# Kernel tuning notes

Hardware: AMD Instinct MI355X
Metric: run time of the kernel (lower is better)

## Reference

```python
import jax, jax.numpy as jnp
import numpy as np

B, T, E = 2, 2048, 2048
H, NOPE, ROPE, VD, KVR, DR = 16, 64, 32, 64, 256, 2
QKD = NOPE + ROPE  # 96
LOWR = KVR // 4    # hypernet low_rank=4 -> 64


def _rope_angles(position, dim):
    # freqs_cis angles: pos * 10000^(-2i/dim), matching torch rotary with theta=10000
    inv = jnp.exp(jnp.arange(0, dim, 2, dtype=jnp.float32) * (-jnp.log(jnp.float32(10000.0)) / dim))
    return position.astype(jnp.float32)[..., None] * inv  # (1, T, dim//2)


def _apply_rotary(x, ang):
    # x: (B,T,H,D); pairs are consecutive elements (view_as_complex semantics)
    x2 = x.reshape(x.shape[:-1] + (-1, 2))
    c = jnp.cos(ang)[:, :, None, :]
    s = jnp.sin(ang)[:, :, None, :]
    xr, xi = x2[..., 0], x2[..., 1]
    return jnp.stack([xr * c - xi * s, xr * s + xi * c], axis=-1).reshape(x.shape)


def _layernorm(x, g, b, eps=1e-5):
    m = jnp.mean(x, axis=-1, keepdims=True)
    v = jnp.var(x, axis=-1, keepdims=True)
    return (x - m) * jax.lax.rsqrt(v + eps) * g + b


def _sinusoid_pe(t, d):
    pos = jnp.arange(t, dtype=jnp.float32)[:, None]
    div = jnp.exp(jnp.arange(0, d, 2, dtype=jnp.float32) * (-jnp.log(jnp.float32(10000.0)) / d))
    pe = jnp.zeros((t, d), dtype=jnp.float32)
    pe = pe.at[:, 0::2].set(jnp.sin(pos * div)).at[:, 1::2].set(jnp.cos(pos * div))
    return pe


def setup_inputs() -> dict:
    key = jax.random.key(0)
    ks = jax.random.split(key, 16)
    sd = 0.02
    return {
        "query": jax.random.normal(ks[0], (B, T, E), jnp.float32),
        "key": jax.random.normal(ks[1], (B, T, E), jnp.float32),
        "value": jax.random.normal(ks[2], (B, T, E), jnp.float32),
        "position": jnp.arange(T, dtype=jnp.int32)[None, :],
        # weights stored transposed for right-multiply (x @ W)
        "wq": jax.random.normal(ks[3], (E, H * QKD), jnp.float32) * sd,
        "wkv_a": jax.random.normal(ks[4], (E, KVR + ROPE), jnp.float32) * sd,
        "kv_gamma": jnp.ones((KVR,), jnp.float32),
        "kv_beta": jnp.zeros((KVR,), jnp.float32),
        # torch layout (H*(NOPE+VD), KVR) kept for faithful view(H,-1,KVR) absorb
        "wkv_b": jax.random.normal(ks[5], (H * (NOPE + VD), KVR), jnp.float32) * sd,
        "wo": jax.random.normal(ks[6], (H * VD, E), jnp.float32) * sd,
        "fc_c_w": jax.random.normal(ks[7], (KVR, LOWR), jnp.float32) * sd,
        "fc_c_b": jnp.zeros((LOWR,), jnp.float32),
        "fc_p_w": jax.random.normal(ks[8], (KVR, LOWR), jnp.float32) * sd,
        "fc_p_b": jnp.zeros((LOWR,), jnp.float32),
    }


def reference(query, key, value, position, wq, wkv_a, kv_gamma, kv_beta, wkv_b, wo,
              fc_c_w, fc_c_b, fc_p_w, fc_p_b):
    bsz, seqlen, _ = query.shape
    # queries: low-rank-free path (q_lora_rank=0)
    q = (query @ wq).reshape(bsz, seqlen, H, QKD)
    q_nope, q_pe = q[..., :NOPE], q[..., NOPE:]
    ang = _rope_angles(position, ROPE)  # (1, T, ROPE//2)
    q_pe = _apply_rotary(q_pe, ang[:, -seqlen:])
    # key/value latent projection
    kv_all = key @ wkv_a  # (B, T, KVR+ROPE)
    kv, k_pe = kv_all[..., :KVR], kv_all[..., KVR:]
    k_pe = _apply_rotary(k_pe[:, :, None, :], ang)[:, :, 0, :]  # (B, T, ROPE)
    kv_norm = _layernorm(kv, kv_gamma, kv_beta)  # (B, T, KVR)
    # hypernetwork temporal downsampling weights (train path, T_input=kv_norm)
    t = -(-seqlen // DR)
    C = jnp.repeat(_sinusoid_pe(t, KVR), DR, axis=0)[:seqlen]  # (T, KVR)
    C2 = C @ fc_c_w + fc_c_b           # (T, LOWR)
    P2 = kv_norm @ fc_p_w + fc_p_b     # (B, T, LOWR)
    W = jax.nn.sigmoid(jnp.einsum('tc,bsc->bts', C2, P2))  # (B, T, T)
    idx = jnp.arange(seqlen)
    chunk = idx // DR
    # chunk mask: cumulative within-chunk causal accumulation
    zero_mask = ((chunk[:, None] == chunk[None, :]) & (idx[None, :] <= idx[:, None])).astype(query.dtype)
    kv_t = jnp.einsum('bts,bsc->btc', W * zero_mask, kv_norm)  # (B, T, KVR)
    # stride-aware causal mask: attend completed chunk-end slots + own in-progress slot
    allowed = (idx[None, :] == idx[:, None]) | ((idx[None, :] < idx[:, None]) & (((idx[None, :] + 1) % DR) == 0))
    attn_mask = jnp.where(allowed, jnp.float32(0.0), jnp.float32(-1e30))
    # absorbed MLA attention
    wb = wkv_b.reshape(H, NOPE + VD, KVR)
    q_abs = jnp.einsum('bshd,hdc->bshc', q_nope, wb[:, :NOPE])  # (B, S, H, KVR)
    scores = (jnp.einsum('bshc,btc->bsht', q_abs, kv_t)
              + jnp.einsum('bshr,btr->bsht', q_pe, k_pe)) * (QKD ** -0.5)
    scores = scores + attn_mask[None, :, None, :]
    attn = jax.nn.softmax(scores, axis=-1)
    x = jnp.einsum('bsht,btc->bshc', attn, kv_t)
    x = jnp.einsum('bshc,hdc->bshd', x, wb[:, NOPE:])  # (B, S, H, VD)
    return x.reshape(bsz, seqlen, H * VD) @ wo
```

## Files before the change

kernel.cpp:

```cpp
#include <hip/hip_runtime.h>
#include <stddef.h>

typedef unsigned short u16;
typedef unsigned short u16x8 __attribute__((ext_vector_type(8)));
typedef short s16x8 __attribute__((ext_vector_type(8)));
typedef float f32x4 __attribute__((ext_vector_type(4)));

#define B_ 2
#define T_ 2048
#define E_ 2048
#define H_ 16

__device__ inline float us2f(u16 u){
  unsigned int i = ((unsigned int)u) << 16;
  return __builtin_bit_cast(float, i);
}
__device__ inline u16 f2us(float f){
  unsigned int x = __builtin_bit_cast(unsigned int, f);
  unsigned int r = (x + 0x7fffu + ((x >> 16) & 1u)) >> 16;
  return (u16)r;
}
__device__ inline f32x4 mfma32(s16x8 a, s16x8 b, f32x4 c){
  return __builtin_amdgcn_mfma_f32_16x16x32_bf16(a, b, c, 0, 0, 0);
}
__device__ inline s16x8 ld8(const u16* p){
  return __builtin_bit_cast(s16x8, *(const u16x8*)p);
}
__device__ inline void gload_lds16(const u16* g, u16* l){
  __builtin_amdgcn_global_load_lds(
      (const __attribute__((address_space(1))) unsigned int*)(g),
      (__attribute__((address_space(3))) unsigned int*)(l), 16, 0, 0);
}

__global__ __launch_bounds__(256) void prep_cvt(
    const float* __restrict__ wq, const float* __restrict__ wkva,
    const float* __restrict__ wo, const float* __restrict__ wkvb,
    const float* __restrict__ query, const float* __restrict__ key_,
    u16* __restrict__ wqT, u16* __restrict__ wkvaT, u16* __restrict__ woT,
    u16* __restrict__ wkvbB, u16* __restrict__ queryB, u16* __restrict__ keyB)
{
  __shared__ float tile[32][33];
  const int bid = blockIdx.x;
  const int tid = threadIdx.x;
  if (bid < 5696) {
    const float* in; u16* out; int R, C, bx, by;
    if (bid < 3072)      { in = wq;   out = wqT;   R = 2048; C = 1536; bx = bid % 48;          by = bid / 48; }
    else if (bid < 3648) { in = wkva; out = wkvaT; R = 2048; C = 288;  bx = (bid-3072) % 9;    by = (bid-3072) / 9; }
    else                 { in = wo;   out = woT;   R = 1024; C = 2048; bx = (bid-3648) % 64;   by = (bid-3648) / 64; }
    int tx = tid & 31, ty = tid >> 5;
    int c0 = bx * 32, r0 = by * 32;
    for (int i = ty; i < 32; i += 8){
      int r = r0 + i, c = c0 + tx;
      tile[i][tx] = (r < R && c < C) ? in[(size_t)r * C + c] : 0.f;
    }
    __syncthreads();
    for (int i = ty; i < 32; i += 8){
      int c = c0 + i, r = r0 + tx;
      if (c < C && r < R) out[(size_t)c * R + r] = f2us(tile[tx][i]);
    }
  } else if (bid < 6208) {
    int i = (bid - 5696) * 1024 + tid * 4;
    f32x4 v = *(const f32x4*)(wkvb + i);
    wkvbB[i]   = f2us(v[0]); wkvbB[i+1] = f2us(v[1]);
    wkvbB[i+2] = f2us(v[2]); wkvbB[i+3] = f2us(v[3]);
  } else {
    const int n_each = 4096 * 2048;
    int idx = (bid - 6208) * 1024 + tid * 4;
    const float* in; u16* out; int i;
    if (idx < n_each){ in = query; out = queryB; i = idx; }
    else             { in = key_;  out = keyB;   i = idx - n_each; }
    if (i + 3 < n_each){
      f32x4 v = *(const f32x4*)(in + i);
      out[i]   = f2us(v[0]); out[i+1] = f2us(v[1]);
      out[i+2] = f2us(v[2]); out[i+3] = f2us(v[3]);
    }
  }
}

__global__ __launch_bounds__(256) void proj2(
    const u16* __restrict__ queryB, const u16* __restrict__ wqT, u16* __restrict__ qp,
    const u16* __restrict__ keyB, const u16* __restrict__ wkvaT, u16* __restrict__ kvall)
{
  __shared__ __align__(16) u16 smem[16384];
  const int bid = blockIdx.x;
  const int tid  = threadIdx.x;
  const int lane = tid & 63;
  const int wid  = tid >> 6;
  const int quad = lane >> 4;
  const int col  = lane & 15;

  if (bid < 768) {
    const int N = 1536, K = 2048, Klen = 1024;
    const int swz = (bid & 7) * 96 + (bid >> 3);
    const int kh  = swz / 384;
    const int rem = swz % 384;
    const int bm = (rem / 12) * 128;
    const int bn = (rem % 12) * 128;
    const int waveM = wid >> 1, waveN = wid & 1;
    u16* As = smem;
    u16* Bs = smem + 8192;

    const int srow = wid * 16 + (lane >> 2);
    const int scol = (lane & 3) * 8;
    const u16* ga = queryB + (size_t)(bm + srow) * K + kh * Klen + scol;
    const u16* gb = wqT    + (size_t)(bn + srow) * K + kh * Klen + scol;
    const size_t rowskip = (size_t)64 * K;
    u16* Cp = qp + (size_t)kh * 4096 * N;

    f32x4 acc[4][4] = {};
    const int nt = Klen >> 5;

    auto STAGE = [&](int buf, int kk){
      u16* la = &As[buf * 4096 + wid * 512];
      u16* lb = &Bs[buf * 4096 + wid * 512];
      gload_lds16(ga + kk,           la);
      gload_lds16(ga + rowskip + kk, la + 2048);
      gload_lds16(gb + kk,           lb);
      gload_lds16(gb + rowskip + kk, lb + 2048);
    };

    STAGE(0, 0);
    asm volatile("s_waitcnt vmcnt(0)" ::: "memory");
    __builtin_amdgcn_s_barrier();
    __builtin_amdgcn_sched_barrier(0);

    int cur = 0;
    for (int it = 0; it < nt; ++it){
      if (it + 1 < nt) STAGE(cur ^ 1, (it + 1) * 32);
      const u16* as = &As[cur * 4096];
      const u16* bs = &Bs[cur * 4096];
      s16x8 af[4], bf[4];
#pragma unroll
      for (int i = 0; i < 4; ++i) af[i] = ld8(&as[(waveM*64 + i*16 + col) * 32 + quad*8]);
#pragma unroll
      for (int i = 0; i < 4; ++i) bf[i] = ld8(&bs[(waveN*64 + i*16 + col) * 32 + quad*8]);
#pragma unroll
      for (int i = 0; i < 4; ++i)
#pragma unroll
        for (int j = 0; j < 4; ++j)
          acc[i][j] = mfma32(af[i], bf[j], acc[i][j]);
      asm volatile("s_waitcnt lgkmcnt(0)" ::: "memory");
      if (it + 1 < nt)
        asm volatile("s_waitcnt vmcnt(0)" ::: "memory");
      __builtin_amdgcn_s_barrier();
      __builtin_amdgcn_sched_barrier(0);
      cur ^= 1;
    }
#pragma unroll
    for (int i = 0; i < 4; ++i)
#pragma unroll
      for (int j = 0; j < 4; ++j)
#pragma unroll
        for (int r = 0; r < 4; ++r) {
          int row = bm + waveM*64 + i*16 + quad*4 + r;
          int c   = bn + waveN*64 + j*16 + col;
          Cp[(size_t)row * N + c] = f2us(acc[i][j][r]);
        }
  } else {
    const int N = 288, K = 2048;
    const int r_ = bid - 768;
    const int bm = (r_ / 5) * 64;
    const int bn = (r_ % 5) * 64;
    const int lr = tid >> 2;
    const int lc = (tid & 3) * 8;
    const int waveM = wid >> 1, waveN = wid & 1;
    u16* As = smem;
    u16* Bs = smem + 2560;

    f32x4 acc[2][2];
    for (int i = 0; i < 2; ++i)
      for (int j = 0; j < 2; ++j)
        acc[i][j] = (f32x4){0.f, 0.f, 0.f, 0.f};

    const u16x8 zero8 = {0,0,0,0,0,0,0,0};
    const bool bok = (bn + lr) < N;
    const u16* arow = keyB  + (size_t)(bm + lr) * K + lc;
    const u16* brow = wkvaT + (size_t)(bn + lr) * K + lc;

    for (int kk = 0; kk < K; kk += 32) {
      u16x8 av = *(const u16x8*)(arow + kk);
      u16x8 bv = bok ? *(const u16x8*)(brow + kk) : zero8;
      __syncthreads();
      *(u16x8*)&As[lr*40 + lc] = av;
      *(u16x8*)&Bs[lr*40 + lc] = bv;
      __syncthreads();
      s16x8 af0 = ld8(&As[(waveM*32 + col)*40 + quad*8]);
      s16x8 af1 = ld8(&As[(waveM*32 + 16 + col)*40 + quad*8]);
      s16x8 bf0 = ld8(&Bs[(waveN*32 + col)*40 + quad*8]);
      s16x8 bf1 = ld8(&Bs[(waveN*32 + 16 + col)*40 + quad*8]);
      acc[0][0] = mfma32(af0, bf0, acc[0][0]);
      acc[0][1] = mfma32(af0, bf1, acc[0][1]);
      acc[1][0] = mfma32(af1, bf0, acc[1][0]);
      acc[1][1] = mfma32(af1, bf1, acc[1][1]);
    }
    for (int am = 0; am < 2; ++am)
      for (int bnn = 0; bnn < 2; ++bnn)
        for (int i = 0; i < 4; ++i) {
          int r = bm + waveM*32 + am*16 + quad*4 + i;
          int c = bn + waveN*32 + bnn*16 + col;
          if (c < N) kvall[(size_t)r * N + c] = f2us(acc[am][bnn][i]);
        }
  }
}

template<int OUT_F32>
__global__ __launch_bounds__(256) void gemm128(const u16* __restrict__ A,
    const u16* __restrict__ Bt, void* __restrict__ Cp, int M, int N, int K, int gx)
{
  __shared__ __align__(16) u16 As[2 * 128 * 32];
  __shared__ __align__(16) u16 Bs[2 * 128 * 32];
  const int lin = blockIdx.x;
  const int cpx = gridDim.x >> 3;
  const int swz = (lin & 7) * cpx + (lin >> 3);
  const int bxi = swz % gx;
  const int byi = swz / gx;
  const int tid  = threadIdx.x;
  const int lane = tid & 63;
  const int wid  = tid >> 6;
  const int quad = lane >> 4;
  const int col  = lane & 15;
  const int bm = byi * 128;
  const int bn = bxi * 128;
  const int waveM = wid >> 1, waveN = wid & 1;

  const int srow = wid * 16 + (lane >> 2);
  const int scol = (lane & 3) * 8;
  const u16* ga = A  + (size_t)(bm + srow) * K + scol;
  const u16* gb = Bt + (size_t)(bn + srow) * K + scol;
  const size_t rowskip = (size_t)64 * K;

  f32x4 acc[4][4] = {};
  const int nt = K >> 5;

  auto STAGE = [&](int buf, int kk){
    u16* la = &As[buf * 4096 + wid * 512];
    u16* lb = &Bs[buf * 4096 + wid * 512];
    gload_lds16(ga + kk,           la);
    gload_lds16(ga + rowskip + kk, la + 2048);
    gload_lds16(gb + kk,           lb);
    gload_lds16(gb + rowskip + kk, lb + 2048);
  };

  STAGE(0, 0);
  asm volatile("s_waitcnt vmcnt(0)" ::: "memory");
  __builtin_amdgcn_s_barrier();
  __builtin_amdgcn_sched_barrier(0);

  int cur = 0;
  for (int it = 0; it < nt; ++it){
    if (it + 1 < nt) STAGE(cur ^ 1, (it + 1) * 32);
    const u16* as = &As[cur * 4096];
    const u16* bs = &Bs[cur * 4096];
    s16x8 af[4], bf[4];
#pragma unroll
    for (int i = 0; i < 4; ++i) af[i] = ld8(&as[(waveM*64 + i*16 + col) * 32 + quad*8]);
#pragma unroll
    for (int i = 0; i < 4; ++i) bf[i] = ld8(&bs[(waveN*64 + i*16 + col) * 32 + quad*8]);
#pragma unroll
    for (int i = 0; i < 4; ++i)
#pragma unroll
      for (int j = 0; j < 4; ++j)
        acc[i][j] = mfma32(af[i], bf[j], acc[i][j]);
    asm volatile("s_waitcnt lgkmcnt(0)" ::: "memory");
    if (it + 1 < nt)
      asm volatile("s_waitcnt vmcnt(0)" ::: "memory");
    __builtin_amdgcn_s_barrier();
    __builtin_amdgcn_sched_barrier(0);
    cur ^= 1;
  }
#pragma unroll
  for (int i = 0; i < 4; ++i)
#pragma unroll
    for (int j = 0; j < 4; ++j)
#pragma unroll
      for (int r = 0; r < 4; ++r) {
        int row = bm + waveM*64 + i*16 + quad*4 + r;
        int c   = bn + waveN*64 + j*16 + col;
        if (OUT_F32) ((float*)Cp)[(size_t)row * N + c] = acc[i][j][r];
        else         ((u16*)Cp)[(size_t)row * N + c]   = f2us(acc[i][j][r]);
      }
}

__global__ __launch_bounds__(256) void mid3(
    const u16* __restrict__ qp, const int* __restrict__ pos, u16* __restrict__ qh,
    const u16* __restrict__ kvall, const float* __restrict__ gamma,
    const float* __restrict__ beta, const float* __restrict__ fcpw,
    const float* __restrict__ fcpb, u16* __restrict__ kvn,
    float* __restrict__ P2, u16* __restrict__ kpe,
    const float* __restrict__ fccw, const float* __restrict__ fccb,
    float* __restrict__ C2)
{
  __shared__ float fsm[520];
  const int bid = blockIdx.x;
  const int tid = threadIdx.x;

  if (bid < 3072) {
    const size_t PS = 4096ull * 1536;
    int idx = bid * 256 + tid;
    int c    = idx % 12;
    int rest = idx / 12;
    int h    = rest & 15;
    int row  = rest >> 4;
    int t    = row & (T_ - 1);
    int b    = row >> 11;
    size_t off = (size_t)row * 1536 + h * 96 + c * 8;
    u16x8 v0 = *(const u16x8*)(qp + off);
    u16x8 v1 = *(const u16x8*)(qp + PS + off);
    u16x8 v;
    if (c < 8) {
#pragma unroll
      for (int k = 0; k < 8; ++k) v[k] = f2us(us2f(v0[k]) + us2f(v1[k]));
    } else {
      int i0 = (c - 8) * 4;
      float pp = (float)pos[t];
#pragma unroll
      for (int k = 0; k < 4; ++k){
        int i = i0 + k;
        float ang = pp * __expf((float)(2*i) * -0.28782313657f);
        float cs = __cosf(ang), sn = __sinf(ang);
        float xr = us2f(v0[2*k])   + us2f(v1[2*k]);
        float xi = us2f(v0[2*k+1]) + us2f(v1[2*k+1]);
        v[2*k]   = f2us(xr * cs - xi * sn);
        v[2*k+1] = f2us(xr * sn + xi * cs);
      }
    }
    u16* dst = qh + ((size_t)(b * 16 + h) * T_ + t) * 96;
    *(u16x8*)(dst + c * 8) = v;
  } else if (bid < 7168) {
    const int row = bid - 3072;
    const int lane = tid & 63, wid = tid >> 6;
    float* kvs   = fsm;
    float* part  = fsm + 256;
    float* redS  = fsm + 512;
    float* redS2 = fsm + 516;
    const u16* src = kvall + (size_t)row * 288;
    float v = us2f(src[tid]);
    float s1 = v, s2 = v * v;
    for (int off = 1; off < 64; off <<= 1){
      s1 += __shfl_xor(s1, off);
      s2 += __shfl_xor(s2, off);
    }
    if (lane == 0){ redS[wid] = s1; redS2[wid] = s2; }
    __syncthreads();
    float S  = redS[0] + redS[1] + redS[2] + redS[3];
    float Q  = redS2[0] + redS2[1] + redS2[2] + redS2[3];
    float mean = S * (1.f / 256.f);
    float var  = Q * (1.f / 256.f) - mean * mean;
    float rstd = rsqrtf(var + 1e-5f);
    float xn = (v - mean) * rstd * gamma[tid] + beta[tid];
    kvs[tid] = xn;
    kvn[(size_t)row * 256 + tid] = f2us(xn);
    __syncthreads();
    {
      int oc = tid & 63, pp = tid >> 6;
      float acc = 0.f;
#pragma unroll 8
      for (int c = pp * 64; c < pp * 64 + 64; ++c)
        acc += kvs[c] * fcpw[c * 64 + oc];
      part[tid] = acc;
    }
    __syncthreads();
    if (tid < 64) {
      P2[(size_t)row * 64 + tid] = fcpb[tid] + part[tid] + part[64 + tid]
                                 + part[128 + tid] + part[192 + tid];
    } else if (tid < 80) {
      int i = tid - 64;
      int t = row & (T_ - 1);
      float ang = (float)pos[t] * __expf((float)(2*i) * -0.28782313657f);
      float c = __cosf(ang), s = __sinf(ang);
      float xr = us2f(src[256 + 2*i]);
      float xi = us2f(src[257 + 2*i]);
      kpe[(size_t)row * 32 + 2*i]     = f2us(xr * c - xi * s);
      kpe[(size_t)row * 32 + 2*i + 1] = f2us(xr * s + xi * c);
    }
  } else {
    const int t = bid - 7168;
    float* pe   = fsm;
    float* part = fsm + 256;
    float p = (float)(t >> 1);
    if (tid < 128){
      float div = __expf((float)(2*tid) * -0.03597789207f);
      float a = p * div;
      pe[2*tid]   = __sinf(a);
      pe[2*tid+1] = __cosf(a);
    }
    __syncthreads();
    {
      int oc = tid & 63, pp = tid >> 6;
      float acc = 0.f;
#pragma unroll 8
      for (int c = pp * 64; c < pp * 64 + 64; ++c)
        acc += pe[c] * fccw[c * 64 + oc];
      part[tid] = acc;
    }
    __syncthreads();
    if (tid < 64)
      C2[t * 64 + tid] = fccb[tid] + part[tid] + part[64 + tid]
                       + part[128 + tid] + part[192 + tid];
  }
}

__global__ __launch_bounds__(256) void kvt_kernel(const float* __restrict__ C2,
    const float* __restrict__ P2, const u16* __restrict__ kvn, u16* __restrict__ kvt)
{
  const int row = blockIdx.x * 4 + (threadIdx.x >> 6);
  const int lane = threadIdx.x & 63;
  const int t = row & (T_ - 1);
  float c2v = C2[t * 64 + lane];
  float da = c2v * P2[(size_t)row * 64 + lane];
  for (int off = 1; off < 64; off <<= 1) da += __shfl_xor(da, off);
  float wtt = 1.f / (1.f + __expf(-da));
  const bool odd = (t & 1);
  float wts = 0.f;
  if (odd){
    float db = c2v * P2[(size_t)(row - 1) * 64 + lane];
    for (int off = 1; off < 64; off <<= 1) db += __shfl_xor(db, off);
    wts = 1.f / (1.f + __expf(-db));
  }
  for (int c = lane; c < 256; c += 64){
    float val = wtt * us2f(kvn[(size_t)row * 256 + c]);
    if (odd) val += wts * us2f(kvn[(size_t)(row - 1) * 256 + c]);
    kvt[(size_t)row * 256 + c] = f2us(val);
  }
}

__global__ __launch_bounds__(256) void vtkc_kernel(const u16* __restrict__ kvb,
    const u16* __restrict__ kpe, u16* __restrict__ Vt, u16* __restrict__ Kc)
{
  __shared__ __align__(16) u16 tile[64][72];
  const int tid = threadIdx.x;
  if (blockIdx.x < 512) {
    const int bid = blockIdx.x;
    const int jt = bid & 15;
    const int h  = (bid >> 4) & 15;
    const int b  = bid >> 8;
    const int jl = tid >> 2;
    const int dseg = (tid & 3) * 16;
    const int j0 = jt * 64;
    {
      int s_ = 2 * (j0 + jl) + 1;
      const u16* src = kvb + ((size_t)(b * T_ + s_)) * 2048 + h * 128 + 64 + dseg;
      *(u16x8*)&tile[jl][dseg]     = *(const u16x8*)(src);
      *(u16x8*)&tile[jl][dseg + 8] = *(const u16x8*)(src + 8);
    }
    __syncthreads();
    const int dl = tid >> 2;
    const int jseg = (tid & 3) * 16;
    u16* dst = Vt + ((size_t)(b * 16 + h) * 64 + dl) * 1024 + j0 + jseg;
    u16x8 o;
    for (int r = 0; r < 8; ++r) o[r] = tile[jseg + r][dl];
    *(u16x8*)dst = o;
    for (int r = 0; r < 8; ++r) o[r] = tile[jseg + 8 + r][dl];
    *(u16x8*)(dst + 8) = o;
  } else {
    int idx = (blockIdx.x - 512) * 256 + tid;
    int c  = idx % 12;
    int j  = (idx / 12) & 1023;
    int bh = idx / (12 * 1024);
    if (bh >= B_ * H_) return;
    int b = bh >> 4, h = bh & 15;
    int t = 2 * j + 1;
    u16x8 v;
    if (c < 8) v = *(const u16x8*)(kvb + ((size_t)(b * T_ + t)) * 2048 + h * 128 + c * 8);
    else       v = *(const u16x8*)(kpe + ((size_t)(b * T_ + t)) * 32 + (c - 8) * 8);
    int kl = j & 63;
    int cs = (c & 12) | ((c & 3) ^ ((kl >> 1) & 3));
    *(u16x8*)(Kc + ((size_t)bh * 1024 + j) * 96 + cs * 8) = v;
  }
}

__global__ __launch_bounds__(256) void attn_kernel(
    const u16* __restrict__ qh, const u16* __restrict__ kvb,
    const u16* __restrict__ kpe, const u16* __restrict__ Kc,
    const u16* __restrict__ Vt, u16* __restrict__ xout)
{
  __shared__ __align__(16) u16 Ks[64 * 96];
  __shared__ __align__(16) u16 Vs[64][72];
  __shared__ __align__(16) u16 pbufA[4][16 * 72];
  const int tid  = threadIdx.x;
  const int wid  = tid >> 6;
  const int lane = tid & 63;
  const int quad = lane >> 4;
  const int col  = lane & 15;
  const int qt   = 31 - (blockIdx.x >> 5);
  const int bh   = blockIdx.x & 31;
  const int b    = bh >> 4;
  const int h    = bh & 15;
  u16* pbuf = pbufA[wid];
  const float scale = 0.10206207262f;
  const u16* KcH = Kc + (size_t)bh * 1024 * 96;
  const u16* VtH = Vt + (size_t)bh * 64 * 1024;
  const int t0 = qt * 64 + wid * 16;
  const int qo = (quad * 8) ^ (((col >> 1) & 3) << 3);

  s16x8 aq0, aq1, aq2;
  {
    const u16* qrow = qh + ((size_t)bh * T_ + t0 + col) * 96;
    aq0 = ld8(qrow + quad * 8);
    aq1 = ld8(qrow + 32 + quad * 8);
    aq2 = ld8(qrow + 64 + quad * 8);
  }
  float sself;
  {
    const int t = t0 + col;
    const u16* qrow = qh + ((size_t)bh * T_ + t) * 96;
    const u16* ka = kvb + ((size_t)(b * T_ + t)) * 2048 + h * 128;
    const u16* kp = kpe + ((size_t)(b * T_ + t)) * 32;
    float a = 0.f;
#pragma unroll
    for (int c = 0; c < 8; ++c){
      u16x8 qv = *(const u16x8*)(qrow + c * 8);
      u16x8 kv = *(const u16x8*)(ka + c * 8);
#pragma unroll
      for (int jj = 0; jj < 8; ++jj) a += us2f(qv[jj]) * us2f(kv[jj]);
    }
#pragma unroll
    for (int c = 0; c < 4; ++c){
      u16x8 qv = *(const u16x8*)(qrow + 64 + c * 8);
      u16x8 kv = *(const u16x8*)(kp + c * 8);
#pragma unroll
      for (int jj = 0; jj < 8; ++jj) a += us2f(qv[jj]) * us2f(kv[jj]);
    }
    sself = a * scale;
  }
  float es[4], lacc[4];
  f32x4 O[4];
#pragma unroll
  for (int i = 0; i < 4; ++i){
    es[i] = __expf(__shfl(sself, quad * 4 + i));
    lacc[i] = 0.f;
  }
#pragma unroll
  for (int nt = 0; nt < 4; ++nt)
#pragma unroll
    for (int i = 0; i < 4; ++i){
      int t = t0 + quad * 4 + i;
      O[nt][i] = es[i] * us2f(kvb[((size_t)(b * T_ + t)) * 2048 + h * 128 + 64 + nt * 16 + col]);
    }

  const int nb = (qt * 32 + 94) >> 6;
  for (int blk = 0; blk < nb; ++blk) {
    const int jb = blk * 64;
    __syncthreads();
    {
      const u16* gk = KcH + (size_t)jb * 96 + (wid * 3) * 512 + lane * 8;
      u16* lk = &Ks[(wid * 3) * 512];
#pragma unroll
      for (int k = 0; k < 3; ++k)
        gload_lds16(gk + k * 512, lk + k * 512);
      int d = tid >> 2, c4 = tid & 3;
      const u16* gv = VtH + (size_t)d * 1024 + jb + c4 * 16;
      u16* lv = &Vs[d][c4 * 16];
      *(u16x8*)(lv)     = *(const u16x8*)(gv);
      *(u16x8*)(lv + 8) = *(const u16x8*)(gv + 8);
    }
    __syncthreads();
#pragma unroll
    for (int cc = 0; cc < 2; ++cc){
      const u16* k0 = &Ks[(cc * 32 + col) * 96];
      const u16* k1 = k0 + 16 * 96;
      f32x4 s0 = {0,0,0,0}, s1 = {0,0,0,0};
      s0 = mfma32(aq0, ld8(k0 + qo), s0);
      s0 = mfma32(aq1, ld8(k0 + 32 + qo), s0);
      s0 = mfma32(aq2, ld8(k0 + 64 + qo), s0);
      s1 = mfma32(aq0, ld8(k1 + qo), s1);
      s1 = mfma32(aq1, ld8(k1 + 32 + qo), s1);
      s1 = mfma32(aq2, ld8(k1 + 64 + qo), s1);
      int key0 = jb + cc * 32 + col;
#pragma unroll
      for (int i = 0; i < 4; ++i){
        int lim = (t0 + quad * 4 + i) >> 1;
        float p0 = (key0 < lim)      ? __expf(s0[i] * scale) : 0.f;
        float p1 = (key0 + 16 < lim) ? __expf(s1[i] * scale) : 0.f;
        lacc[i] += p0 + p1;
        pbuf[(quad * 4 + i) * 72 + cc * 32 + col]      = f2us(p0);
        pbuf[(quad * 4 + i) * 72 + cc * 32 + 16 + col] = f2us(p1);
      }
    }
    asm volatile("s_waitcnt lgkmcnt(0)" ::: "memory");
    __builtin_amdgcn_sched_barrier(0);
#pragma unroll
    for (int cc = 0; cc < 2; ++cc){
      s16x8 pf = ld8(&pbuf[col * 72 + cc * 32 + quad * 8]);
#pragma unroll
      for (int nt = 0; nt < 4; ++nt)
        O[nt] = mfma32(pf, ld8(&Vs[nt * 16 + col][cc * 32 + quad * 8]), O[nt]);
    }
  }
#pragma unroll
  for (int i = 0; i < 4; ++i){
    float l = lacc[i];
    l += __shfl_xor(l, 1);
    l += __shfl_xor(l, 2);
    l += __shfl_xor(l, 4);
    l += __shfl_xor(l, 8);
    lacc[i] = es[i] + l;
  }
#pragma unroll
  for (int nt = 0; nt < 4; ++nt)
#pragma unroll
    for (int i = 0; i < 4; ++i){
      int t = t0 + quad * 4 + i;
      xout[((size_t)(b * T_ + t)) * 1024 + h * 64 + nt * 16 + col] = f2us(O[nt][i] / lacc[i]);
    }
}

extern "C" void kernel_launch(void* const* d_in, const int* in_sizes, int n_in,
                              void* d_out, int out_size, void* d_ws, size_t ws_size,
                              hipStream_t stream)
{
  (void)in_sizes; (void)n_in; (void)out_size; (void)ws_size;
  const float* query = (const float*)d_in[0];
  const float* key_  = (const float*)d_in[1];
  const int*   pos   = (const int*)d_in[3];
  const float* wq    = (const float*)d_in[4];
  const float* wkva  = (const float*)d_in[5];
  const float* gamma = (const float*)d_in[6];
  const float* beta  = (const float*)d_in[7];
  const float* wkvb  = (const float*)d_in[8];
  const float* wo    = (const float*)d_in[9];
  const float* fccw  = (const float*)d_in[10];
  const float* fccb  = (const float*)d_in[11];
  const float* fcpw  = (const float*)d_in[12];
  const float* fcpb  = (const float*)d_in[13];

  char* p = (char*)d_ws;
  auto alloc = [&](size_t bytes) -> void* {
    void* r = (void*)p;
    p += (bytes + 255) & ~(size_t)255;
    return r;
  };
  u16* wqT    = (u16*)alloc(1536ull * 2048 * 2);
  u16* wkvaT  = (u16*)alloc(288ull  * 2048 * 2);
  u16* woT    = (u16*)alloc(2048ull * 1024 * 2);
  u16* wkvbB  = (u16*)alloc(2048ull * 256 * 2);
  u16* queryB = (u16*)alloc(4096ull * 2048 * 2);
  u16* keyB   = (u16*)alloc(4096ull * 2048 * 2);
  u16* qp     = (u16*)alloc(2ull * 4096 * 1536 * 2);
  u16* qh     = (u16*)alloc(65536ull * 96 * 2);
  u16* kvall  = (u16*)alloc(4096ull * 288 * 2);
  u16* kvn    = (u16*)alloc(4096ull * 256 * 2);
  u16* kpe    = (u16*)alloc(4096ull * 32 * 2);
  float* P2   = (float*)alloc(4096ull * 64 * 4);
  float* C2   = (float*)alloc(2048ull * 64 * 4);
  u16* kvt    = (u16*)alloc(4096ull * 256 * 2);
  u16* kvb    = (u16*)alloc(4096ull * 2048 * 2);
  char* q8 = (char*)qp;
  u16* Kc = (u16*)q8;
  u16* Vt = (u16*)(q8 + ((32ull*1024*96*2 + 255) & ~255ull));
  u16* x  = (u16*)(q8 + ((32ull*1024*96*2 + 255) & ~255ull)
                      + ((2048ull*1024*2   + 255) & ~255ull));

  prep_cvt<<<22592, 256, 0, stream>>>(wq, wkva, wo, wkvb, query, key_,
                                      wqT, wkvaT, woT, wkvbB, queryB, keyB);
  proj2<<<1088, 256, 0, stream>>>(queryB, wqT, qp, keyB, wkvaT, kvall);
  mid3<<<9216, 256, 0, stream>>>(qp, pos, qh, kvall, gamma, beta, fcpw, fcpb,
                                 kvn, P2, kpe, fccw, fccb, C2);
  kvt_kernel<<<1024, 256, 0, stream>>>(C2, P2, kvn, kvt);

  gemm128<0><<<512, 256, 0, stream>>>(kvt, wkvbB, kvb, 4096, 2048, 256, 16);
  vtkc_kernel<<<2048, 256, 0, stream>>>(kvb, kpe, Vt, Kc);
  attn_kernel<<<1024, 256, 0, stream>>>(qh, kvb, kpe, Kc, Vt, x);

  gemm128<1><<<512, 256, 0, stream>>>(x, woT, d_out, 4096, 2048, 1024, 16);
}
```

Before: 337.3 us.

## Split-K the kv_a projection into four fp32 partials and interleave blocks with q projection

The small key×wkv_a GEMM used to run 320 blocks, each looping over the full K=2048. It now uses a 4-way split-K with fp32 partial outputs, which mid3 sums when it loads. Block ids are remapped so q-projection tiles and kv tiles interleave across the grid, the q tiles get an M-grouped ordering, MFMA sections get higher wave priority, and the kv loop prefetches the next global tile into registers. This targets the long tail from the serial kv blocks, at the cost of extra fp32 partial traffic and summation work in mid3.

```diff
diff --git a/kernel.cpp b/kernel.cpp
--- a/kernel.cpp
+++ b/kernel.cpp
@@ -79,7 +79,7 @@
 
 __global__ __launch_bounds__(256) void proj2(
     const u16* __restrict__ queryB, const u16* __restrict__ wqT, u16* __restrict__ qp,
-    const u16* __restrict__ keyB, const u16* __restrict__ wkvaT, u16* __restrict__ kvall)
+    const u16* __restrict__ keyB, const u16* __restrict__ wkvaT, float* __restrict__ kvp)
 {
   __shared__ __align__(16) u16 smem[16384];
   const int bid = blockIdx.x;
@@ -88,14 +88,19 @@
   const int wid  = tid >> 6;
   const int quad = lane >> 4;
   const int col  = lane & 15;
-
-  if (bid < 768) {
+  const int g  = bid >> 3;
+  const int e  = bid & 7;
+  const int gm = g & 7;
+
+  if (gm < 3) {
+    const int id = e * 96 + (g >> 3) * 3 + gm;
+    const int kh   = id / 384;
+    const int r2   = id % 384;
+    const int bmHi = r2 / 48;
+    const int r3   = r2 % 48;
+    const int bn = (r3 >> 2) * 128;
+    const int bm = (bmHi * 4 + (r3 & 3)) * 128;
     const int N = 1536, K = 2048, Klen = 1024;
-    const int swz = (bid & 7) * 96 + (bid >> 3);
-    const int kh  = swz / 384;
-    const int rem = swz % 384;
-    const int bm = (rem / 12) * 128;
-    const int bn = (rem % 12) * 128;
     const int waveM = wid >> 1, waveN = wid & 1;
     u16* As = smem;
     u16* Bs = smem + 8192;
@@ -134,11 +139,13 @@
       for (int i = 0; i < 4; ++i) af[i] = ld8(&as[(waveM*64 + i*16 + col) * 32 + quad*8]);
 #pragma unroll
       for (int i = 0; i < 4; ++i) bf[i] = ld8(&bs[(waveN*64 + i*16 + col) * 32 + quad*8]);
+      __builtin_amdgcn_s_setprio(1);
 #pragma unroll
       for (int i = 0; i < 4; ++i)
 #pragma unroll
         for (int j = 0; j < 4; ++j)
           acc[i][j] = mfma32(af[i], bf[j], acc[i][j]);
+      __builtin_amdgcn_s_setprio(0);
       asm volatile("s_waitcnt lgkmcnt(0)" ::: "memory");
       if (it + 1 < nt)
         asm volatile("s_waitcnt vmcnt(0)" ::: "memory");
@@ -157,10 +164,12 @@
           Cp[(size_t)row * N + c] = f2us(acc[i][j][r]);
         }
   } else {
-    const int N = 288, K = 2048;
-    const int r_ = bid - 768;
-    const int bm = (r_ / 5) * 64;
-    const int bn = (r_ % 5) * 64;
+    const int id = e * 160 + (g >> 3) * 5 + (gm - 3);
+    const int kh = id / 320;
+    const int r  = id % 320;
+    const int bm = (r / 5) * 64;
+    const int bn = (r % 5) * 64;
+    const int N = 288, K = 2048, Klen = 512;
     const int lr = tid >> 2;
     const int lc = (tid & 3) * 8;
     const int waveM = wid >> 1, waveN = wid & 1;
@@ -174,15 +183,20 @@
 
     const u16x8 zero8 = {0,0,0,0,0,0,0,0};
     const bool bok = (bn + lr) < N;
-    const u16* arow = keyB  + (size_t)(bm + lr) * K + lc;
-    const u16* brow = wkvaT + (size_t)(bn + lr) * K + lc;
-
-    for (int kk = 0; kk < K; kk += 32) {
-      u16x8 av = *(const u16x8*)(arow + kk);
-      u16x8 bv = bok ? *(const u16x8*)(brow + kk) : zero8;
+    const u16* arow = keyB  + (size_t)(bm + lr) * K + kh * Klen + lc;
+    const u16* brow = wkvaT + (size_t)(bn + lr) * K + kh * Klen + lc;
+    float* Cp = kvp + (size_t)kh * 4096 * N;
+
+    u16x8 av = *(const u16x8*)(arow);
+    u16x8 bv = bok ? *(const u16x8*)(brow) : zero8;
+    for (int kk = 0; kk < Klen; kk += 32) {
       __syncthreads();
       *(u16x8*)&As[lr*40 + lc] = av;
       *(u16x8*)&Bs[lr*40 + lc] = bv;
+      if (kk + 32 < Klen){
+        av = *(const u16x8*)(arow + kk + 32);
+        bv = bok ? *(const u16x8*)(brow + kk + 32) : zero8;
+      }
       __syncthreads();
       s16x8 af0 = ld8(&As[(waveM*32 + col)*40 + quad*8]);
       s16x8 af1 = ld8(&As[(waveM*32 + 16 + col)*40 + quad*8]);
@@ -196,9 +210,9 @@
     for (int am = 0; am < 2; ++am)
       for (int bnn = 0; bnn < 2; ++bnn)
         for (int i = 0; i < 4; ++i) {
-          int r = bm + waveM*32 + am*16 + quad*4 + i;
-          int c = bn + waveN*32 + bnn*16 + col;
-          if (c < N) kvall[(size_t)r * N + c] = f2us(acc[am][bnn][i]);
+          int rr = bm + waveM*32 + am*16 + quad*4 + i;
+          int c  = bn + waveN*32 + bnn*16 + col;
+          if (c < N) Cp[(size_t)rr * N + c] = acc[am][bnn][i];
         }
   }
 }
@@ -283,7 +297,7 @@
 
 __global__ __launch_bounds__(256) void mid3(
     const u16* __restrict__ qp, const int* __restrict__ pos, u16* __restrict__ qh,
-    const u16* __restrict__ kvall, const float* __restrict__ gamma,
+    const float* __restrict__ kvp, const float* __restrict__ gamma,
     const float* __restrict__ beta, const float* __restrict__ fcpw,
     const float* __restrict__ fcpb, u16* __restrict__ kvn,
     float* __restrict__ P2, u16* __restrict__ kpe,
@@ -329,12 +343,13 @@
   } else if (bid < 7168) {
     const int row = bid - 3072;
     const int lane = tid & 63, wid = tid >> 6;
+    const size_t PSk = 4096ull * 288;
     float* kvs   = fsm;
     float* part  = fsm + 256;
     float* redS  = fsm + 512;
     float* redS2 = fsm + 516;
-    const u16* src = kvall + (size_t)row * 288;
-    float v = us2f(src[tid]);
+    const float* src = kvp + (size_t)row * 288;
+    float v = (src[tid] + src[PSk + tid]) + (src[2*PSk + tid] + src[3*PSk + tid]);
     float s1 = v, s2 = v * v;
     for (int off = 1; off < 64; off <<= 1){
       s1 += __shfl_xor(s1, off);
@@ -368,8 +383,10 @@
       int t = row & (T_ - 1);
       float ang = (float)pos[t] * __expf((float)(2*i) * -0.28782313657f);
       float c = __cosf(ang), s = __sinf(ang);
-      float xr = us2f(src[256 + 2*i]);
-      float xi = us2f(src[257 + 2*i]);
+      float xr = (src[256 + 2*i] + src[PSk + 256 + 2*i])
+               + (src[2*PSk + 256 + 2*i] + src[3*PSk + 256 + 2*i]);
+      float xi = (src[257 + 2*i] + src[PSk + 257 + 2*i])
+               + (src[2*PSk + 257 + 2*i] + src[3*PSk + 257 + 2*i]);
       kpe[(size_t)row * 32 + 2*i]     = f2us(xr * c - xi * s);
       kpe[(size_t)row * 32 + 2*i + 1] = f2us(xr * s + xi * c);
     }
@@ -637,8 +654,8 @@
   u16* queryB = (u16*)alloc(4096ull * 2048 * 2);
   u16* keyB   = (u16*)alloc(4096ull * 2048 * 2);
   u16* qp     = (u16*)alloc(2ull * 4096 * 1536 * 2);
+  float* kvp  = (float*)alloc(4ull * 4096 * 288 * 4);
   u16* qh     = (u16*)alloc(65536ull * 96 * 2);
-  u16* kvall  = (u16*)alloc(4096ull * 288 * 2);
   u16* kvn    = (u16*)alloc(4096ull * 256 * 2);
   u16* kpe    = (u16*)alloc(4096ull * 32 * 2);
   float* P2   = (float*)alloc(4096ull * 64 * 4);
@@ -653,8 +670,8 @@
 
   prep_cvt<<<22592, 256, 0, stream>>>(wq, wkva, wo, wkvb, query, key_,
                                       wqT, wkvaT, woT, wkvbB, queryB, keyB);
-  proj2<<<1088, 256, 0, stream>>>(queryB, wqT, qp, keyB, wkvaT, kvall);
-  mid3<<<9216, 256, 0, stream>>>(qp, pos, qh, kvall, gamma, beta, fcpw, fcpb,
+  proj2<<<2048, 256, 0, stream>>>(queryB, wqT, qp, keyB, wkvaT, kvp);
+  mid3<<<9216, 256, 0, stream>>>(qp, pos, qh, kvp, gamma, beta, fcpw, fcpb,
                                  kvn, P2, kpe, fccw, fccb, C2);
   kvt_kernel<<<1024, 256, 0, stream>>>(C2, P2, kvn, kvt);
 
```

Result: no change. 332.5 us (-1.4%).
